# Optimization experiments

Measured on AMD Instinct MI355X. Metric: run time of the kernel, lower is better.

Reference implementation:

```python
import jax, jax.numpy as jnp
import numpy as np

NUM_PPR_NODES = 262144
BATCH = 4096
K = NUM_PPR_NODES // BATCH  # ppr neighbors per batch node
F_IN, H, C = 256, 512, 64


def setup_inputs() -> dict:
    key = jax.random.key(0)
    ks = jax.random.split(key, 6)
    X = jax.random.normal(ks[0], (NUM_PPR_NODES, F_IN), dtype=jnp.float32)
    ppr_scores = jax.random.uniform(ks[1], (NUM_PPR_NODES,), dtype=jnp.float32)
    # sorted batch ids; last element == BATCH-1 so dim_size = ppr_idx[-1]+1 = BATCH
    ppr_idx = jnp.repeat(jnp.arange(BATCH, dtype=jnp.int64), K)
    s1 = 1.0 / np.sqrt(F_IN)
    s2 = 1.0 / np.sqrt(H)
    Wa = jax.random.uniform(ks[2], (F_IN, H), jnp.float32, -s1, s1)
    Wb = jax.random.uniform(ks[3], (H, H), jnp.float32, -s2, s2)
    Wc = jax.random.uniform(ks[4], (H, H), jnp.float32, -s2, s2)
    Wd = jax.random.uniform(ks[5], (H, C), jnp.float32, -s2, s2)
    return {"X": X, "ppr_scores": ppr_scores, "ppr_idx": ppr_idx,
            "Wa": Wa, "Wb": Wb, "Wc": Wc, "Wd": Wd}


def reference(X, ppr_scores, ppr_idx, Wa, Wb, Wc, Wd):
    # embedding MLP (dropout inactive at eval): Linear -> ReLU -> Linear, no bias
    emb = jax.nn.relu(X @ Wa) @ Wb                      # [N, H]
    # weighted scatter-sum over ppr neighborhoods
    weighted = emb * ppr_scores[:, None]                # [N, H]
    agg = jax.ops.segment_sum(weighted, ppr_idx, num_segments=BATCH)  # [B, H]
    # logit MLP: Linear -> ReLU -> Linear, no bias
    logits = jax.nn.relu(agg @ Wc) @ Wd                 # [B, C]
    return logits
```

## Files before the change

### kernel.cpp

```cpp
#include <hip/hip_runtime.h>

typedef short bs8 __attribute__((ext_vector_type(8)));
typedef float fx4 __attribute__((ext_vector_type(4)));

__device__ __forceinline__ unsigned short f2bf(float f) {
    unsigned u = __builtin_bit_cast(unsigned, f);
    u += 0x7FFFu + ((u >> 16) & 1u);
    return (unsigned short)(u >> 16);
}

__device__ __forceinline__ bs8 load_cvt8(const float* p) {
    fx4 u = *(const fx4*)p;
    fx4 v = *(const fx4*)(p + 4);
    bs8 r;
    r[0] = (short)f2bf(u[0]); r[1] = (short)f2bf(u[1]);
    r[2] = (short)f2bf(u[2]); r[3] = (short)f2bf(u[3]);
    r[4] = (short)f2bf(v[0]); r[5] = (short)f2bf(v[1]);
    r[6] = (short)f2bf(v[2]); r[7] = (short)f2bf(v[3]);
    return r;
}

__global__ void pack_b(const float* __restrict__ src, unsigned short* __restrict__ dst,
                       int KN, int N) {
    const int l = threadIdx.x;
    const int lr = l & 15, lg = l >> 4;
    const int bid = blockIdx.x;
    const int cf = bid / KN, kc = bid % KN;
    const int col  = cf * 16 + lr;
    const int krow = kc * 32 + lg * 8;
    const size_t ob = ((size_t)bid * 64 + l) * 8;
    #pragma unroll
    for (int j = 0; j < 8; ++j)
        dst[ob + j] = f2bf(src[(size_t)(krow + j) * N + col]);
}

__global__ __launch_bounds__(256) void wbc_gemm(const float* __restrict__ Wb,
                                                const float* __restrict__ Wc,
                                                float* __restrict__ Wbc) {
    __shared__ float As[32][33];
    __shared__ float Bs[32][33];
    const int tx = threadIdx.x & 15, ty = threadIdx.x >> 4;
    const int i0 = blockIdx.y * 32, j0 = blockIdx.x * 32;
    float c00 = 0.f, c01 = 0.f, c10 = 0.f, c11 = 0.f;
    for (int k0 = 0; k0 < 512; k0 += 32) {
        for (int t = threadIdx.x; t < 1024; t += 256) {
            int r = t >> 5, c = t & 31;
            As[r][c] = Wb[(size_t)(i0 + r) * 512 + k0 + c];
            Bs[r][c] = Wc[(size_t)(k0 + r) * 512 + j0 + c];
        }
        __syncthreads();
        #pragma unroll
        for (int k = 0; k < 32; ++k) {
            float a0 = As[ty * 2][k], a1 = As[ty * 2 + 1][k];
            float b0 = Bs[k][tx * 2], b1 = Bs[k][tx * 2 + 1];
            c00 += a0 * b0; c01 += a0 * b1; c10 += a1 * b0; c11 += a1 * b1;
        }
        __syncthreads();
    }
    Wbc[(size_t)(i0 + ty * 2) * 512 + j0 + tx * 2]         = c00;
    Wbc[(size_t)(i0 + ty * 2) * 512 + j0 + tx * 2 + 1]     = c01;
    Wbc[(size_t)(i0 + ty * 2 + 1) * 512 + j0 + tx * 2]     = c10;
    Wbc[(size_t)(i0 + ty * 2 + 1) * 512 + j0 + tx * 2 + 1] = c11;
}

__global__ __launch_bounds__(256, 2) void k1_fused(
    const float* __restrict__ X, const float* __restrict__ scores,
    const bs8* __restrict__ WaP, unsigned short* __restrict__ aggH) {
    __shared__ unsigned short xt[64 * 256];

    const int tid = threadIdx.x;
    const int seg = blockIdx.x;
    const size_t row0 = (size_t)seg * 64;

    #pragma unroll
    for (int it = 0; it < 8; ++it) {
        const int flat = it * 2048 + tid * 8;
        const int r = flat >> 8, c = flat & 255;
        bs8 v = load_cvt8(X + (row0 + r) * 256 + c);
        int byte = r * 512 + c * 2;
        byte ^= (r & 7) << 4;
        *(bs8*)((char*)xt + byte) = v;
    }
    __syncthreads();

    const int w = tid >> 6, l = tid & 63;
    const int lr = l & 15, lg = l >> 4;

    #pragma unroll 1
    for (int ci = 0; ci < 2; ++ci) {
        const int cc = w * 2 + ci;
        fx4 acc[4][4];
        #pragma unroll
        for (int mf = 0; mf < 4; ++mf)
            #pragma unroll
            for (int nf = 0; nf < 4; ++nf)
                acc[mf][nf] = (fx4){0.f, 0.f, 0.f, 0.f};

        #pragma unroll
        for (int kc = 0; kc < 8; ++kc) {
            bs8 b[4];
            #pragma unroll
            for (int nf = 0; nf < 4; ++nf)
                b[nf] = WaP[((cc * 4 + nf) * 8 + kc) * 64 + l];
            bs8 a[4];
            #pragma unroll
            for (int mf = 0; mf < 4; ++mf) {
                const int row = mf * 16 + lr;
                int byte = row * 512 + kc * 64 + lg * 16;
                byte ^= (row & 7) << 4;
                a[mf] = *(const bs8*)((const char*)xt + byte);
            }
            #pragma unroll
            for (int mf = 0; mf < 4; ++mf)
                #pragma unroll
                for (int nf = 0; nf < 4; ++nf)
                    acc[mf][nf] = __builtin_amdgcn_mfma_f32_16x16x32_bf16(
                        a[mf], b[nf], acc[mf][nf], 0, 0, 0);
        }

        float sc0[4][4];
        #pragma unroll
        for (int mf = 0; mf < 4; ++mf) {
            fx4 s = *(const fx4*)(scores + row0 + mf * 16 + lg * 4);
            sc0[mf][0] = s[0]; sc0[mf][1] = s[1]; sc0[mf][2] = s[2]; sc0[mf][3] = s[3];
        }
        #pragma unroll
        for (int nf = 0; nf < 4; ++nf) {
            float p = 0.f;
            #pragma unroll
            for (int mf = 0; mf < 4; ++mf)
                #pragma unroll
                for (int r = 0; r < 4; ++r) {
                    float v = acc[mf][nf][r];
                    v = v > 0.f ? v : 0.f;
                    p += v * sc0[mf][r];
                }
            p += __shfl_xor(p, 16, 64);
            p += __shfl_xor(p, 32, 64);
            if (lg == 0)
                aggH[(size_t)seg * 512 + cc * 64 + nf * 16 + lr] = f2bf(p);
        }
    }
}

__global__ __launch_bounds__(256) void k2_gemm(
    const unsigned short* __restrict__ aggH, const bs8* __restrict__ WbcP,
    unsigned short* __restrict__ T) {
    const int tid = threadIdx.x;
    const int w = tid >> 6, l = tid & 63, lr = l & 15, lg = l >> 4;
    const int gw = blockIdx.x * 4 + w;
    const int rg = gw >> 3, cg = gw & 7;
    const int r0 = rg * 64, c0 = cg * 64;

    fx4 acc[4][4];
    #pragma unroll
    for (int mf = 0; mf < 4; ++mf)
        #pragma unroll
        for (int nf = 0; nf < 4; ++nf)
            acc[mf][nf] = (fx4){0.f, 0.f, 0.f, 0.f};

    #pragma unroll 1
    for (int kc = 0; kc < 16; ++kc) {
        bs8 a[4], b[4];
        #pragma unroll
        for (int mf = 0; mf < 4; ++mf)
            a[mf] = *(const bs8*)(aggH + (size_t)(r0 + mf * 16 + lr) * 512 + kc * 32 + lg * 8);
        #pragma unroll
        for (int nf = 0; nf < 4; ++nf)
            b[nf] = WbcP[((cg * 4 + nf) * 16 + kc) * 64 + l];
        #pragma unroll
        for (int mf = 0; mf < 4; ++mf)
            #pragma unroll
            for (int nf = 0; nf < 4; ++nf)
                acc[mf][nf] = __builtin_amdgcn_mfma_f32_16x16x32_bf16(
                    a[mf], b[nf], acc[mf][nf], 0, 0, 0);
    }
    #pragma unroll
    for (int mf = 0; mf < 4; ++mf)
        #pragma unroll
        for (int nf = 0; nf < 4; ++nf)
            #pragma unroll
            for (int r = 0; r < 4; ++r) {
                float v = fmaxf(acc[mf][nf][r], 0.f);
                T[(size_t)(r0 + mf * 16 + lg * 4 + r) * 512 + c0 + nf * 16 + lr] = f2bf(v);
            }
}

__global__ __launch_bounds__(256) void k3_gemm(
    const unsigned short* __restrict__ T, const bs8* __restrict__ WdP,
    float* __restrict__ out) {
    const int tid = threadIdx.x;
    const int w = tid >> 6, l = tid & 63, lr = l & 15, lg = l >> 4;
    const int gw = blockIdx.x * 4 + w;
    const int r0 = gw * 64;

    fx4 acc[4][4];
    #pragma unroll
    for (int mf = 0; mf < 4; ++mf)
        #pragma unroll
        for (int nf = 0; nf < 4; ++nf)
            acc[mf][nf] = (fx4){0.f, 0.f, 0.f, 0.f};

    #pragma unroll 1
    for (int kc = 0; kc < 16; ++kc) {
        bs8 a[4], b[4];
        #pragma unroll
        for (int mf = 0; mf < 4; ++mf)
            a[mf] = *(const bs8*)(T + (size_t)(r0 + mf * 16 + lr) * 512 + kc * 32 + lg * 8);
        #pragma unroll
        for (int nf = 0; nf < 4; ++nf)
            b[nf] = WdP[(nf * 16 + kc) * 64 + l];
        #pragma unroll
        for (int mf = 0; mf < 4; ++mf)
            #pragma unroll
            for (int nf = 0; nf < 4; ++nf)
                acc[mf][nf] = __builtin_amdgcn_mfma_f32_16x16x32_bf16(
                    a[mf], b[nf], acc[mf][nf], 0, 0, 0);
    }
    #pragma unroll
    for (int mf = 0; mf < 4; ++mf)
        #pragma unroll
        for (int nf = 0; nf < 4; ++nf)
            #pragma unroll
            for (int r = 0; r < 4; ++r)
                out[(size_t)(r0 + mf * 16 + lg * 4 + r) * 64 + nf * 16 + lr] = acc[mf][nf][r];
}

extern "C" void kernel_launch(void* const* d_in, const int* in_sizes, int n_in,
                              void* d_out, int out_size, void* d_ws, size_t ws_size,
                              hipStream_t stream) {
    const float* X  = (const float*)d_in[0];
    const float* sc = (const float*)d_in[1];
    const float* Wa = (const float*)d_in[3];
    const float* Wb = (const float*)d_in[4];
    const float* Wc = (const float*)d_in[5];
    const float* Wd = (const float*)d_in[6];
    float* out = (float*)d_out;

    char* ws = (char*)d_ws;
    unsigned short* WaP  = (unsigned short*)(ws + 0);
    unsigned short* WbcP = (unsigned short*)(ws + 262144);
    unsigned short* WdP  = (unsigned short*)(ws + 786432);
    float*          Wbc  = (float*)         (ws + 851968);
    unsigned short* aggH = (unsigned short*)(ws + 1900544);
    unsigned short* T    = (unsigned short*)(ws + 6094848);

    pack_b<<<dim3(32 * 8),  dim3(64), 0, stream>>>(Wa,  WaP,  8,  512);
    wbc_gemm<<<dim3(16, 16), dim3(256), 0, stream>>>(Wb, Wc, Wbc);
    pack_b<<<dim3(32 * 16), dim3(64), 0, stream>>>(Wbc, WbcP, 16, 512);
    pack_b<<<dim3(4 * 16),  dim3(64), 0, stream>>>(Wd,  WdP,  16, 64);

    k1_fused<<<dim3(4096), dim3(256), 0, stream>>>(X, sc, (const bs8*)WaP, aggH);
    k2_gemm<<<dim3(128),   dim3(256), 0, stream>>>(aggH, (const bs8*)WbcP, T);
    k3_gemm<<<dim3(16),    dim3(256), 0, stream>>>(T, (const bs8*)WdP, out);
}
```

Baseline: 189.5 us.

## Make k1 persistent with register-resident Wa half and double-buffered X staging

```diff
diff --git a/kernel.cpp b/kernel.cpp
--- a/kernel.cpp
+++ b/kernel.cpp
@@ -66,80 +66,98 @@
 __global__ __launch_bounds__(256, 2) void k1_fused(
     const float* __restrict__ X, const float* __restrict__ scores,
     const bs8* __restrict__ WaP, unsigned short* __restrict__ aggH) {
-    __shared__ unsigned short xt[64 * 256];
+    __shared__ unsigned short xt[2][16384];
 
     const int tid = threadIdx.x;
-    const int seg = blockIdx.x;
-    const size_t row0 = (size_t)seg * 64;
-
-    #pragma unroll
-    for (int it = 0; it < 8; ++it) {
-        const int flat = it * 2048 + tid * 8;
-        const int r = flat >> 8, c = flat & 255;
-        bs8 v = load_cvt8(X + (row0 + r) * 256 + c);
-        int byte = r * 512 + c * 2;
-        byte ^= (r & 7) << 4;
-        *(bs8*)((char*)xt + byte) = v;
-    }
-    __syncthreads();
-
     const int w = tid >> 6, l = tid & 63;
     const int lr = l & 15, lg = l >> 4;
 
+    const int bid = blockIdx.x;
+    const int xcd = bid & 7;
+    const int slot = bid >> 3;
+    const int h = slot & 1;
+    const int chunk = xcd * 32 + (slot >> 1);
+    const int seg0 = chunk * 16;
+
+    bs8 bfr[4][8];
+    #pragma unroll
+    for (int j = 0; j < 4; ++j)
+        #pragma unroll
+        for (int kc = 0; kc < 8; ++kc)
+            bfr[j][kc] = WaP[(size_t)(((h * 16 + w * 4 + j) * 8 + kc) * 64) + l];
+
+    auto stage = [&](int seg, unsigned short* buf) {
+        const size_t row0 = (size_t)seg * 64;
+        #pragma unroll
+        for (int it = 0; it < 8; ++it) {
+            const int flat = it * 2048 + tid * 8;
+            const int r = flat >> 8, c = flat & 255;
+            bs8 v = load_cvt8(X + (row0 + r) * 256 + c);
+            int byte = r * 512 + c * 2;
+            byte ^= (r & 7) << 4;
+            *(bs8*)((char*)buf + byte) = v;
+        }
+    };
+
+    stage(seg0, xt[0]);
+
     #pragma unroll 1
-    for (int ci = 0; ci < 2; ++ci) {
-        const int cc = w * 2 + ci;
+    for (int s = 0; s < 16; ++s) {
+        __syncthreads();
+        const int seg = seg0 + s;
+        const unsigned short* buf = xt[s & 1];
+
         fx4 acc[4][4];
         #pragma unroll
-        for (int mf = 0; mf < 4; ++mf)
-            #pragma unroll
-            for (int nf = 0; nf < 4; ++nf)
-                acc[mf][nf] = (fx4){0.f, 0.f, 0.f, 0.f};
+        for (int j = 0; j < 4; ++j)
+            #pragma unroll
+            for (int mf = 0; mf < 4; ++mf)
+                acc[j][mf] = (fx4){0.f, 0.f, 0.f, 0.f};
 
         #pragma unroll
         for (int kc = 0; kc < 8; ++kc) {
-            bs8 b[4];
-            #pragma unroll
-            for (int nf = 0; nf < 4; ++nf)
-                b[nf] = WaP[((cc * 4 + nf) * 8 + kc) * 64 + l];
             bs8 a[4];
             #pragma unroll
             for (int mf = 0; mf < 4; ++mf) {
                 const int row = mf * 16 + lr;
-                int byte = row * 512 + kc * 64 + lg * 16;
-                byte ^= (row & 7) << 4;
-                a[mf] = *(const bs8*)((const char*)xt + byte);
+                const int x = row * 512 + kc * 64 + lg * 16;
+                a[mf] = *(const bs8*)((const char*)buf + (x ^ ((row & 7) << 4)));
             }
             #pragma unroll
-            for (int mf = 0; mf < 4; ++mf)
+            for (int j = 0; j < 4; ++j)
                 #pragma unroll
-                for (int nf = 0; nf < 4; ++nf)
-                    acc[mf][nf] = __builtin_amdgcn_mfma_f32_16x16x32_bf16(
-                        a[mf], b[nf], acc[mf][nf], 0, 0, 0);
-        }
-
-        float sc0[4][4];
+                for (int mf = 0; mf < 4; ++mf)
+                    acc[j][mf] = __builtin_amdgcn_mfma_f32_16x16x32_bf16(
+                        a[mf], bfr[j][kc], acc[j][mf], 0, 0, 0);
+        }
+
+        const size_t row0 = (size_t)seg * 64;
+        float sct[4][4];
         #pragma unroll
         for (int mf = 0; mf < 4; ++mf) {
-            fx4 s = *(const fx4*)(scores + row0 + mf * 16 + lg * 4);
-            sc0[mf][0] = s[0]; sc0[mf][1] = s[1]; sc0[mf][2] = s[2]; sc0[mf][3] = s[3];
-        }
-        #pragma unroll
-        for (int nf = 0; nf < 4; ++nf) {
+            fx4 sv = *(const fx4*)(scores + row0 + mf * 16 + lg * 4);
+            sct[mf][0] = sv[0]; sct[mf][1] = sv[1];
+            sct[mf][2] = sv[2]; sct[mf][3] = sv[3];
+        }
+        #pragma unroll
+        for (int j = 0; j < 4; ++j) {
             float p = 0.f;
             #pragma unroll
             for (int mf = 0; mf < 4; ++mf)
                 #pragma unroll
                 for (int r = 0; r < 4; ++r) {
-                    float v = acc[mf][nf][r];
+                    float v = acc[j][mf][r];
                     v = v > 0.f ? v : 0.f;
-                    p += v * sc0[mf][r];
+                    p += v * sct[mf][r];
                 }
             p += __shfl_xor(p, 16, 64);
             p += __shfl_xor(p, 32, 64);
             if (lg == 0)
-                aggH[(size_t)seg * 512 + cc * 64 + nf * 16 + lr] = f2bf(p);
-        }
+                aggH[(size_t)seg * 512 + h * 256 + w * 64 + j * 16 + lr] = f2bf(p);
+        }
+
+        if (s + 1 < 16)
+            stage(seg + 1, xt[(s + 1) & 1]);
     }
 }
 
@@ -250,7 +268,7 @@
     pack_b<<<dim3(32 * 16), dim3(64), 0, stream>>>(Wbc, WbcP, 16, 512);
     pack_b<<<dim3(4 * 16),  dim3(64), 0, stream>>>(Wd,  WdP,  16, 64);
 
-    k1_fused<<<dim3(4096), dim3(256), 0, stream>>>(X, sc, (const bs8*)WaP, aggH);
-    k2_gemm<<<dim3(128),   dim3(256), 0, stream>>>(aggH, (const bs8*)WbcP, T);
-    k3_gemm<<<dim3(16),    dim3(256), 0, stream>>>(T, (const bs8*)WdP, out);
-}
+    k1_fused<<<dim3(512), dim3(256), 0, stream>>>(X, sc, (const bs8*)WaP, aggH);
+    k2_gemm<<<dim3(128),  dim3(256), 0, stream>>>(aggH, (const bs8*)WbcP, T);
+    k3_gemm<<<dim3(16),   dim3(256), 0, stream>>>(T, (const bs8*)WdP, out);
+}
```

Result: slower. 319.7 us (+68.8%).
